# Kernel tuning notes

Measured on AMD Instinct MI355X. Metric: run time of the kernel, lower is better.

Reference implementation:

```python
import jax, jax.numpy as jnp
import numpy as np

N_ENTITIES = 100000
N_EDGES = 1250000
N_RELATIONS = 32
D = 64


def setup_inputs() -> dict:
    key = jax.random.key(0)
    k1, k2, k3, k4 = jax.random.split(key, 4)
    entity_emb = jax.random.normal(k1, (N_ENTITIES, D), dtype=jnp.float32)
    edge_index = jax.random.randint(k2, (2, N_EDGES), 0, N_ENTITIES, dtype=jnp.int64)
    edge_type = jax.random.randint(k3, (N_EDGES,), 0, N_RELATIONS, dtype=jnp.int64)
    weight = jax.random.normal(k4, (N_RELATIONS, D), dtype=jnp.float32)
    return {"entity_emb": entity_emb, "edge_index": edge_index,
            "edge_type": edge_type, "weight": weight}


def reference(entity_emb, edge_index, edge_type, weight):
    n_entities = entity_emb.shape[0]
    head, tail = edge_index[0], edge_index[1]
    # gather tail entity embeddings and relation embeddings, elementwise multiply
    neigh_relation_emb = entity_emb[tail] * weight[edge_type]  # [E, D]
    # scatter_mean by head index
    sums = jax.ops.segment_sum(neigh_relation_emb, head, num_segments=n_entities)
    counts = jax.ops.segment_sum(jnp.ones((head.shape[0],), dtype=entity_emb.dtype),
                                 head, num_segments=n_entities)
    entity_agg = sums / jnp.maximum(counts, 1.0)[:, None]  # empty segments -> 0
    return entity_agg
```

## Files before the change

### kernel.cpp

```cpp
#include <hip/hip_runtime.h>

#define D 64
#define BIN_SHIFT 7
#define BIN_SIZE 128
#define MAX_BINS 1024
#define BINCAP 2560
#define K1_THREADS 512
#define K1_EPT 10
#define K1_EPB (K1_THREADS * K1_EPT)
#define K2_THREADS 512
#define NREL 32


__device__ __forceinline__ float bf2f(unsigned short u) {
    union { unsigned i; float f; } x; x.i = ((unsigned)u) << 16; return x.f;
}

__global__ void cvt_kernel(const float* __restrict__ emb,
                           unsigned short* __restrict__ emb16,
                           int* __restrict__ binCount, int nbins, long n4) {
    long i = (long)blockIdx.x * blockDim.x + threadIdx.x;
    if (i < (long)nbins) binCount[i] = 0;
    if (i >= n4) return;
    float4 v = ((const float4*)emb)[i];
    ushort4 o;
    unsigned b;
    b = __float_as_uint(v.x); o.x = (unsigned short)((b + 0x7FFF + ((b >> 16) & 1)) >> 16);
    b = __float_as_uint(v.y); o.y = (unsigned short)((b + 0x7FFF + ((b >> 16) & 1)) >> 16);
    b = __float_as_uint(v.z); o.z = (unsigned short)((b + 0x7FFF + ((b >> 16) & 1)) >> 16);
    b = __float_as_uint(v.w); o.w = (unsigned short)((b + 0x7FFF + ((b >> 16) & 1)) >> 16);
    ((ushort4*)emb16)[i] = o;
}

__global__ void __launch_bounds__(K1_THREADS)
bin_sort_kernel(const int* __restrict__ head,
                const int* __restrict__ tail,
                const int* __restrict__ etype,
                int* __restrict__ binCount,
                unsigned* __restrict__ recs,
                int nbins, int n_edges) {
    __shared__ unsigned srec[K1_EPB];
    __shared__ int hist[MAX_BINS];
    __shared__ int base[MAX_BINS + 1];
    __shared__ int cur[MAX_BINS];
    __shared__ int gpos[MAX_BINS];
    __shared__ int tmp[K1_THREADS];
    __shared__ unsigned short binof[K1_EPB];

    int tid = threadIdx.x;
    for (int b = tid; b < MAX_BINS; b += K1_THREADS) hist[b] = 0;
    __syncthreads();

    long blockBase = (long)blockIdx.x * K1_EPB;
    int nvalid = (int)(((long)n_edges - blockBase < (long)K1_EPB)
                       ? ((long)n_edges - blockBase) : (long)K1_EPB);

    unsigned rv[K1_EPT]; int bv[K1_EPT];
#pragma unroll
    for (int k = 0; k < K1_EPT; k++) {
        long e = blockBase + (long)k * K1_THREADS + tid;
        if (e < n_edges) {
            int h = head[e];
            bv[k] = h >> BIN_SHIFT;
            rv[k] = (unsigned)tail[e] | ((unsigned)etype[e] << 17)
                  | ((unsigned)(h & (BIN_SIZE - 1)) << 22);
            atomicAdd(&hist[bv[k]], 1);
        } else bv[k] = -1;
    }
    __syncthreads();

    int s0 = hist[2 * tid], s1 = hist[2 * tid + 1];
    tmp[tid] = s0 + s1;
    __syncthreads();
    for (int s = 1; s < K1_THREADS; s <<= 1) {
        int x = (tid >= s) ? tmp[tid - s] : 0;
        __syncthreads();
        tmp[tid] += x;
        __syncthreads();
    }
    int pairExcl = tmp[tid] - (s0 + s1);
    base[2 * tid] = pairExcl;          cur[2 * tid] = pairExcl;
    base[2 * tid + 1] = pairExcl + s0; cur[2 * tid + 1] = pairExcl + s0;
    if (tid == K1_THREADS - 1) base[MAX_BINS] = tmp[tid];
    __syncthreads();

    for (int b = tid; b < nbins; b += K1_THREADS) {
        int c = hist[b];
        gpos[b] = (c > 0) ? atomicAdd(&binCount[b], c) : 0;
    }
    __syncthreads();

#pragma unroll
    for (int k = 0; k < K1_EPT; k++) {
        if (bv[k] >= 0) {
            int p = atomicAdd(&cur[bv[k]], 1);
            srec[p] = rv[k];
        }
    }
    __syncthreads();

    for (int b = tid; b < nbins; b += K1_THREADS) {
        int j0 = base[b], j1 = base[b + 1];
        for (int j = j0; j < j1; j++) binof[j] = (unsigned short)b;
    }
    __syncthreads();

    for (int i = tid; i < nvalid; i += K1_THREADS) {
        int b = binof[i];
        int off = gpos[b] + (i - base[b]);
        if (off < BINCAP)
            recs[(long)b * BINCAP + off] = srec[i];
    }
}

__global__ void __launch_bounds__(K2_THREADS)
aggregate_bin_kernel(const unsigned short* __restrict__ emb16,
                     const float* __restrict__ weight,
                     const unsigned* __restrict__ recs,
                     const int* __restrict__ binCount,
                     float* __restrict__ out, int n_ent) {
    __shared__ unsigned raw[BINCAP];
    __shared__ unsigned sorted[BINCAP + 16];
    __shared__ float wlds[NREL * D];
    __shared__ int hist[BIN_SIZE];
    __shared__ int off[BIN_SIZE];
    __shared__ int cur[BIN_SIZE];

    int tid = threadIdx.x;
    int b = blockIdx.x;
    int n = min(binCount[b], BINCAP);

    for (int i = tid; i < BINCAP + 16; i += K2_THREADS) sorted[i] = 0u;
    for (int i = tid; i < NREL * D; i += K2_THREADS) wlds[i] = weight[i];
    if (tid < BIN_SIZE) hist[tid] = 0;
    __syncthreads();

    const unsigned* gr = recs + (long)b * BINCAP;
    for (int i = tid; i < n; i += K2_THREADS) {
        unsigned q = gr[i];
        raw[i] = q;
        atomicAdd(&hist[(q >> 22) & 127], 1);
    }
    __syncthreads();

    int v = 0;
    if (tid < BIN_SIZE) { v = hist[tid]; off[tid] = v; }
    __syncthreads();
    for (int s = 1; s < BIN_SIZE; s <<= 1) {
        int x = 0;
        if (tid < BIN_SIZE && tid >= s) x = off[tid - s];
        __syncthreads();
        if (tid < BIN_SIZE) off[tid] += x;
        __syncthreads();
    }
    if (tid < BIN_SIZE) { off[tid] -= v; cur[tid] = off[tid]; }
    __syncthreads();

    for (int i = tid; i < n; i += K2_THREADS) {
        unsigned q = raw[i];
        int p = atomicAdd(&cur[(q >> 22) & 127], 1);
        sorted[p] = q;
    }
    __syncthreads();

    int lane = tid & 63;
    int wave = tid >> 6;
    int g = lane >> 4;
    int c = lane & 15;
    int hbase = b << BIN_SHIFT;

    for (int hl = wave; hl < BIN_SIZE; hl += 8) {
        if (hbase + hl >= n_ent) break;
        int o = off[hl];
        int deg = hist[hl];
        float4 acc = make_float4(0.f, 0.f, 0.f, 0.f);
        for (int i = 0; i < deg; i += 16) {
            int e0 = i + g, e1 = i + 4 + g, e2 = i + 8 + g, e3 = i + 12 + g;
            unsigned q0 = sorted[o + e0];
            unsigned q1 = sorted[o + e1];
            unsigned q2 = sorted[o + e2];
            unsigned q3 = sorted[o + e3];
            ushort4 u0 = *(const ushort4*)&emb16[(long)(q0 & 0x1FFFF) * D + c * 4];
            ushort4 u1 = *(const ushort4*)&emb16[(long)(q1 & 0x1FFFF) * D + c * 4];
            ushort4 u2 = *(const ushort4*)&emb16[(long)(q2 & 0x1FFFF) * D + c * 4];
            ushort4 u3 = *(const ushort4*)&emb16[(long)(q3 & 0x1FFFF) * D + c * 4];
            float4 w0 = *(const float4*)&wlds[(((q0 >> 17) & 31) << 6) + c * 4];
            float4 w1 = *(const float4*)&wlds[(((q1 >> 17) & 31) << 6) + c * 4];
            float4 w2 = *(const float4*)&wlds[(((q2 >> 17) & 31) << 6) + c * 4];
            float4 w3 = *(const float4*)&wlds[(((q3 >> 17) & 31) << 6) + c * 4];
            float m0 = (e0 < deg) ? 1.f : 0.f;
            float m1 = (e1 < deg) ? 1.f : 0.f;
            float m2 = (e2 < deg) ? 1.f : 0.f;
            float m3 = (e3 < deg) ? 1.f : 0.f;
            acc.x += m0 * bf2f(u0.x) * w0.x; acc.y += m0 * bf2f(u0.y) * w0.y;
            acc.z += m0 * bf2f(u0.z) * w0.z; acc.w += m0 * bf2f(u0.w) * w0.w;
            acc.x += m1 * bf2f(u1.x) * w1.x; acc.y += m1 * bf2f(u1.y) * w1.y;
            acc.z += m1 * bf2f(u1.z) * w1.z; acc.w += m1 * bf2f(u1.w) * w1.w;
            acc.x += m2 * bf2f(u2.x) * w2.x; acc.y += m2 * bf2f(u2.y) * w2.y;
            acc.z += m2 * bf2f(u2.z) * w2.z; acc.w += m2 * bf2f(u2.w) * w2.w;
            acc.x += m3 * bf2f(u3.x) * w3.x; acc.y += m3 * bf2f(u3.y) * w3.y;
            acc.z += m3 * bf2f(u3.z) * w3.z; acc.w += m3 * bf2f(u3.w) * w3.w;
        }
        acc.x += __shfl_xor(acc.x, 16); acc.y += __shfl_xor(acc.y, 16);
        acc.z += __shfl_xor(acc.z, 16); acc.w += __shfl_xor(acc.w, 16);
        acc.x += __shfl_xor(acc.x, 32); acc.y += __shfl_xor(acc.y, 32);
        acc.z += __shfl_xor(acc.z, 32); acc.w += __shfl_xor(acc.w, 32);
        if (g == 0) {
            float inv = 1.f / fmaxf((float)deg, 1.f);
            *(float4*)&out[(long)(hbase + hl) * D + c * 4] =
                make_float4(acc.x * inv, acc.y * inv, acc.z * inv, acc.w * inv);
        }
    }
}

__global__ void fb_scatter(const float* __restrict__ emb, const int* __restrict__ head,
                           const int* __restrict__ tail, const int* __restrict__ etype,
                           const float* __restrict__ weight, float* __restrict__ out,
                           float* __restrict__ cnt, int n_edges) {
    int gtid = blockIdx.x * blockDim.x + threadIdx.x;
    int e = gtid >> 6, lane = threadIdx.x & 63;
    if (e >= n_edges) return;
    int h = head[e], t = tail[e], r = etype[e];
    atomicAdd(&out[(long)h * D + lane], emb[(long)t * D + lane] * weight[r * D + lane]);
    if (lane == 0) atomicAdd(&cnt[h], 1.0f);
}
__global__ void fb_divide(float* __restrict__ out, const float* __restrict__ cnt, int n) {
    int i = blockIdx.x * blockDim.x + threadIdx.x;
    if (i < n) out[i] = out[i] / fmaxf(cnt[i >> 6], 1.0f);
}


extern "C" void kernel_launch(void* const* d_in, const int* in_sizes, int n_in,
                              void* d_out, int out_size, void* d_ws, size_t ws_size,
                              hipStream_t stream) {
    const float* emb    = (const float*)d_in[0];
    const int*   eidx   = (const int*)  d_in[1];
    const int*   etype  = (const int*)  d_in[2];
    const float* weight = (const float*)d_in[3];
    float* out = (float*)d_out;

    int n_edges = in_sizes[2];
    int n_ent   = out_size / D;
    const int* head = eidx;
    const int* tail = eidx + n_edges;

    int nbins = (n_ent + BIN_SIZE - 1) >> BIN_SHIFT;
    size_t recs_bytes = sizeof(int) * ((size_t)nbins * BINCAP);
    size_t cnt_bytes  = sizeof(int) * (size_t)nbins;
    size_t emb16_off  = (cnt_bytes + recs_bytes + 15) & ~((size_t)15);
    size_t need = emb16_off + (size_t)n_ent * D * sizeof(unsigned short);
    long mean_load = (n_ent > 0) ? ((long)n_edges * BIN_SIZE / n_ent) : 0;
    bool ok = (n_ent <= 131072) && (nbins <= MAX_BINS) && (ws_size >= need) &&
              (mean_load + 700 <= BINCAP);

    if (ok) {
        int* binCount  = (int*)d_ws;
        unsigned* recs = (unsigned*)(binCount + nbins);
        unsigned short* emb16 = (unsigned short*)((char*)d_ws + emb16_off);

        long n4 = (long)n_ent * D / 4;
        cvt_kernel<<<(int)((n4 + 255) / 256), 256, 0, stream>>>(
            emb, emb16, binCount, nbins, n4);

        int nblocks = (n_edges + K1_EPB - 1) / K1_EPB;
        bin_sort_kernel<<<nblocks, K1_THREADS, 0, stream>>>(
            head, tail, etype, binCount, recs, nbins, n_edges);

        aggregate_bin_kernel<<<nbins, K2_THREADS, 0, stream>>>(
            emb16, weight, recs, binCount, out, n_ent);
    } else {
        float* cnt = (float*)d_ws;
        hipMemsetAsync(out, 0, (size_t)out_size * sizeof(float), stream);
        hipMemsetAsync(cnt, 0, (size_t)n_ent * sizeof(float), stream);
        long tt = (long)n_edges * 64;
        fb_scatter<<<(int)((tt + 255) / 256), 256, 0, stream>>>(
            emb, head, tail, etype, weight, out, cnt, n_edges);
        fb_divide<<<(out_size + 255) / 256, 256, 0, stream>>>(out, cnt, out_size);
    }
}
```

Baseline: 152.5 us.

## Process two heads per wave, use wave-shuffle scan, trim LDS zeroing

The aggregation loop now has each wave handle two head nodes at once, issuing eight gathers per iteration instead of four, so more memory requests are in flight. The LDS prefix scan over the 128-entry histogram is replaced by a single-wave shuffle scan, removing the many block-wide barriers. Only the 16 padding slots after the valid records are zeroed instead of the whole sorted buffer, and launch bounds now request 4 blocks per CU. The costs are higher register pressure and wasted work when the two paired heads have unequal degrees.

```diff
diff --git a/kernel.cpp b/kernel.cpp
--- a/kernel.cpp
+++ b/kernel.cpp
@@ -113,7 +113,7 @@
     }
 }
 
-__global__ void __launch_bounds__(K2_THREADS)
+__global__ void __launch_bounds__(K2_THREADS, 4)
 aggregate_bin_kernel(const unsigned short* __restrict__ emb16,
                      const float* __restrict__ weight,
                      const unsigned* __restrict__ recs,
@@ -130,7 +130,7 @@
     int b = blockIdx.x;
     int n = min(binCount[b], BINCAP);
 
-    for (int i = tid; i < BINCAP + 16; i += K2_THREADS) sorted[i] = 0u;
+    if (tid < 16) sorted[n + tid] = 0u;
     for (int i = tid; i < NREL * D; i += K2_THREADS) wlds[i] = weight[i];
     if (tid < BIN_SIZE) hist[tid] = 0;
     __syncthreads();
@@ -143,17 +143,25 @@
     }
     __syncthreads();
 
-    int v = 0;
-    if (tid < BIN_SIZE) { v = hist[tid]; off[tid] = v; }
-    __syncthreads();
-    for (int s = 1; s < BIN_SIZE; s <<= 1) {
-        int x = 0;
-        if (tid < BIN_SIZE && tid >= s) x = off[tid - s];
-        __syncthreads();
-        if (tid < BIN_SIZE) off[tid] += x;
-        __syncthreads();
-    }
-    if (tid < BIN_SIZE) { off[tid] -= v; cur[tid] = off[tid]; }
+    int lane = tid & 63;
+    int wave = tid >> 6;
+
+    if (wave == 0) {
+        int h0 = hist[lane];
+        int h1 = hist[64 + lane];
+        int s0 = h0, s1 = h1;
+#pragma unroll
+        for (int s = 1; s < 64; s <<= 1) {
+            int t0 = __shfl_up(s0, s);
+            int t1 = __shfl_up(s1, s);
+            if (lane >= s) { s0 += t0; s1 += t1; }
+        }
+        int tot0 = __shfl(s0, 63);
+        int e0 = s0 - h0;
+        int e1 = tot0 + s1 - h1;
+        off[lane] = e0;      cur[lane] = e0;
+        off[64 + lane] = e1; cur[64 + lane] = e1;
+    }
     __syncthreads();
 
     for (int i = tid; i < n; i += K2_THREADS) {
@@ -163,52 +171,88 @@
     }
     __syncthreads();
 
-    int lane = tid & 63;
-    int wave = tid >> 6;
     int g = lane >> 4;
-    int c = lane & 15;
+    int c4 = (lane & 15) << 2;
     int hbase = b << BIN_SHIFT;
-
-    for (int hl = wave; hl < BIN_SIZE; hl += 8) {
-        if (hbase + hl >= n_ent) break;
-        int o = off[hl];
-        int deg = hist[hl];
-        float4 acc = make_float4(0.f, 0.f, 0.f, 0.f);
-        for (int i = 0; i < deg; i += 16) {
+    int nclamp = n + 15;
+
+#pragma unroll 1
+    for (int j = 0; j < 8; ++j) {
+        int hA = wave + (j << 4);
+        int hB = hA + 8;
+        int oA = off[hA], dA = hist[hA];
+        int oB = off[hB], dB = hist[hB];
+        int dmax = max(dA, dB);
+        float4 accA = make_float4(0.f, 0.f, 0.f, 0.f);
+        float4 accB = make_float4(0.f, 0.f, 0.f, 0.f);
+        for (int i = 0; i < dmax; i += 16) {
             int e0 = i + g, e1 = i + 4 + g, e2 = i + 8 + g, e3 = i + 12 + g;
-            unsigned q0 = sorted[o + e0];
-            unsigned q1 = sorted[o + e1];
-            unsigned q2 = sorted[o + e2];
-            unsigned q3 = sorted[o + e3];
-            ushort4 u0 = *(const ushort4*)&emb16[(long)(q0 & 0x1FFFF) * D + c * 4];
-            ushort4 u1 = *(const ushort4*)&emb16[(long)(q1 & 0x1FFFF) * D + c * 4];
-            ushort4 u2 = *(const ushort4*)&emb16[(long)(q2 & 0x1FFFF) * D + c * 4];
-            ushort4 u3 = *(const ushort4*)&emb16[(long)(q3 & 0x1FFFF) * D + c * 4];
-            float4 w0 = *(const float4*)&wlds[(((q0 >> 17) & 31) << 6) + c * 4];
-            float4 w1 = *(const float4*)&wlds[(((q1 >> 17) & 31) << 6) + c * 4];
-            float4 w2 = *(const float4*)&wlds[(((q2 >> 17) & 31) << 6) + c * 4];
-            float4 w3 = *(const float4*)&wlds[(((q3 >> 17) & 31) << 6) + c * 4];
-            float m0 = (e0 < deg) ? 1.f : 0.f;
-            float m1 = (e1 < deg) ? 1.f : 0.f;
-            float m2 = (e2 < deg) ? 1.f : 0.f;
-            float m3 = (e3 < deg) ? 1.f : 0.f;
-            acc.x += m0 * bf2f(u0.x) * w0.x; acc.y += m0 * bf2f(u0.y) * w0.y;
-            acc.z += m0 * bf2f(u0.z) * w0.z; acc.w += m0 * bf2f(u0.w) * w0.w;
-            acc.x += m1 * bf2f(u1.x) * w1.x; acc.y += m1 * bf2f(u1.y) * w1.y;
-            acc.z += m1 * bf2f(u1.z) * w1.z; acc.w += m1 * bf2f(u1.w) * w1.w;
-            acc.x += m2 * bf2f(u2.x) * w2.x; acc.y += m2 * bf2f(u2.y) * w2.y;
-            acc.z += m2 * bf2f(u2.z) * w2.z; acc.w += m2 * bf2f(u2.w) * w2.w;
-            acc.x += m3 * bf2f(u3.x) * w3.x; acc.y += m3 * bf2f(u3.y) * w3.y;
-            acc.z += m3 * bf2f(u3.z) * w3.z; acc.w += m3 * bf2f(u3.w) * w3.w;
-        }
-        acc.x += __shfl_xor(acc.x, 16); acc.y += __shfl_xor(acc.y, 16);
-        acc.z += __shfl_xor(acc.z, 16); acc.w += __shfl_xor(acc.w, 16);
-        acc.x += __shfl_xor(acc.x, 32); acc.y += __shfl_xor(acc.y, 32);
-        acc.z += __shfl_xor(acc.z, 32); acc.w += __shfl_xor(acc.w, 32);
-        if (g == 0) {
-            float inv = 1.f / fmaxf((float)deg, 1.f);
-            *(float4*)&out[(long)(hbase + hl) * D + c * 4] =
-                make_float4(acc.x * inv, acc.y * inv, acc.z * inv, acc.w * inv);
+            unsigned qa0 = sorted[min(oA + e0, nclamp)];
+            unsigned qa1 = sorted[min(oA + e1, nclamp)];
+            unsigned qa2 = sorted[min(oA + e2, nclamp)];
+            unsigned qa3 = sorted[min(oA + e3, nclamp)];
+            unsigned qb0 = sorted[min(oB + e0, nclamp)];
+            unsigned qb1 = sorted[min(oB + e1, nclamp)];
+            unsigned qb2 = sorted[min(oB + e2, nclamp)];
+            unsigned qb3 = sorted[min(oB + e3, nclamp)];
+            ushort4 ua0 = *(const ushort4*)&emb16[((long)(qa0 & 0x1FFFF) << 6) + c4];
+            ushort4 ua1 = *(const ushort4*)&emb16[((long)(qa1 & 0x1FFFF) << 6) + c4];
+            ushort4 ua2 = *(const ushort4*)&emb16[((long)(qa2 & 0x1FFFF) << 6) + c4];
+            ushort4 ua3 = *(const ushort4*)&emb16[((long)(qa3 & 0x1FFFF) << 6) + c4];
+            ushort4 ub0 = *(const ushort4*)&emb16[((long)(qb0 & 0x1FFFF) << 6) + c4];
+            ushort4 ub1 = *(const ushort4*)&emb16[((long)(qb1 & 0x1FFFF) << 6) + c4];
+            ushort4 ub2 = *(const ushort4*)&emb16[((long)(qb2 & 0x1FFFF) << 6) + c4];
+            ushort4 ub3 = *(const ushort4*)&emb16[((long)(qb3 & 0x1FFFF) << 6) + c4];
+            float4 wa0 = *(const float4*)&wlds[(((qa0 >> 17) & 31) << 6) + c4];
+            float4 wa1 = *(const float4*)&wlds[(((qa1 >> 17) & 31) << 6) + c4];
+            float4 wa2 = *(const float4*)&wlds[(((qa2 >> 17) & 31) << 6) + c4];
+            float4 wa3 = *(const float4*)&wlds[(((qa3 >> 17) & 31) << 6) + c4];
+            float4 wb0 = *(const float4*)&wlds[(((qb0 >> 17) & 31) << 6) + c4];
+            float4 wb1 = *(const float4*)&wlds[(((qb1 >> 17) & 31) << 6) + c4];
+            float4 wb2 = *(const float4*)&wlds[(((qb2 >> 17) & 31) << 6) + c4];
+            float4 wb3 = *(const float4*)&wlds[(((qb3 >> 17) & 31) << 6) + c4];
+            float ma0 = (e0 < dA) ? 1.f : 0.f;
+            float ma1 = (e1 < dA) ? 1.f : 0.f;
+            float ma2 = (e2 < dA) ? 1.f : 0.f;
+            float ma3 = (e3 < dA) ? 1.f : 0.f;
+            float mb0 = (e0 < dB) ? 1.f : 0.f;
+            float mb1 = (e1 < dB) ? 1.f : 0.f;
+            float mb2 = (e2 < dB) ? 1.f : 0.f;
+            float mb3 = (e3 < dB) ? 1.f : 0.f;
+            accA.x += ma0 * bf2f(ua0.x) * wa0.x; accA.y += ma0 * bf2f(ua0.y) * wa0.y;
+            accA.z += ma0 * bf2f(ua0.z) * wa0.z; accA.w += ma0 * bf2f(ua0.w) * wa0.w;
+            accA.x += ma1 * bf2f(ua1.x) * wa1.x; accA.y += ma1 * bf2f(ua1.y) * wa1.y;
+            accA.z += ma1 * bf2f(ua1.z) * wa1.z; accA.w += ma1 * bf2f(ua1.w) * wa1.w;
+            accA.x += ma2 * bf2f(ua2.x) * wa2.x; accA.y += ma2 * bf2f(ua2.y) * wa2.y;
+            accA.z += ma2 * bf2f(ua2.z) * wa2.z; accA.w += ma2 * bf2f(ua2.w) * wa2.w;
+            accA.x += ma3 * bf2f(ua3.x) * wa3.x; accA.y += ma3 * bf2f(ua3.y) * wa3.y;
+            accA.z += ma3 * bf2f(ua3.z) * wa3.z; accA.w += ma3 * bf2f(ua3.w) * wa3.w;
+            accB.x += mb0 * bf2f(ub0.x) * wb0.x; accB.y += mb0 * bf2f(ub0.y) * wb0.y;
+            accB.z += mb0 * bf2f(ub0.z) * wb0.z; accB.w += mb0 * bf2f(ub0.w) * wb0.w;
+            accB.x += mb1 * bf2f(ub1.x) * wb1.x; accB.y += mb1 * bf2f(ub1.y) * wb1.y;
+            accB.z += mb1 * bf2f(ub1.z) * wb1.z; accB.w += mb1 * bf2f(ub1.w) * wb1.w;
+            accB.x += mb2 * bf2f(ub2.x) * wb2.x; accB.y += mb2 * bf2f(ub2.y) * wb2.y;
+            accB.z += mb2 * bf2f(ub2.z) * wb2.z; accB.w += mb2 * bf2f(ub2.w) * wb2.w;
+            accB.x += mb3 * bf2f(ub3.x) * wb3.x; accB.y += mb3 * bf2f(ub3.y) * wb3.y;
+            accB.z += mb3 * bf2f(ub3.z) * wb3.z; accB.w += mb3 * bf2f(ub3.w) * wb3.w;
+        }
+        accA.x += __shfl_xor(accA.x, 16); accA.y += __shfl_xor(accA.y, 16);
+        accA.z += __shfl_xor(accA.z, 16); accA.w += __shfl_xor(accA.w, 16);
+        accA.x += __shfl_xor(accA.x, 32); accA.y += __shfl_xor(accA.y, 32);
+        accA.z += __shfl_xor(accA.z, 32); accA.w += __shfl_xor(accA.w, 32);
+        accB.x += __shfl_xor(accB.x, 16); accB.y += __shfl_xor(accB.y, 16);
+        accB.z += __shfl_xor(accB.z, 16); accB.w += __shfl_xor(accB.w, 16);
+        accB.x += __shfl_xor(accB.x, 32); accB.y += __shfl_xor(accB.y, 32);
+        accB.z += __shfl_xor(accB.z, 32); accB.w += __shfl_xor(accB.w, 32);
+        if (g == 0 && hbase + hA < n_ent) {
+            float inv = 1.f / fmaxf((float)dA, 1.f);
+            *(float4*)&out[((long)(hbase + hA) << 6) + c4] =
+                make_float4(accA.x * inv, accA.y * inv, accA.z * inv, accA.w * inv);
+        }
+        if (g == 0 && hbase + hB < n_ent) {
+            float inv = 1.f / fmaxf((float)dB, 1.f);
+            *(float4*)&out[((long)(hbase + hB) << 6) + c4] =
+                make_float4(accB.x * inv, accB.y * inv, accB.z * inv, accB.w * inv);
         }
     }
 }
```

Result: slower. 156.4 us (+2.6%).

## Software-pipeline head aggregation with double-buffered prefetch and wave-level scan

Applied to the files above, without the earlier changes.

The aggregation kernel now prefetches the first 16 edges' embedding and weight data for the next head while computing the current head, using two register sets A and B. This is meant to hide gather latency across heads. The 128-entry prefix scan now runs in a single wave with shuffles instead of a barrier-heavy LDS scan, and only the 16 tail slots of the sorted array are zeroed instead of the whole buffer. Launch bounds are set to request two blocks per CU. The extra live registers for the prefetch could raise register pressure or cause spills.

```diff
diff --git a/kernel.cpp b/kernel.cpp
--- a/kernel.cpp
+++ b/kernel.cpp
@@ -113,7 +113,7 @@
     }
 }
 
-__global__ void __launch_bounds__(K2_THREADS)
+__global__ void __launch_bounds__(K2_THREADS, 2)
 aggregate_bin_kernel(const unsigned short* __restrict__ emb16,
                      const float* __restrict__ weight,
                      const unsigned* __restrict__ recs,
@@ -130,7 +130,7 @@
     int b = blockIdx.x;
     int n = min(binCount[b], BINCAP);
 
-    for (int i = tid; i < BINCAP + 16; i += K2_THREADS) sorted[i] = 0u;
+    if (tid < 16) sorted[n + tid] = 0u;
     for (int i = tid; i < NREL * D; i += K2_THREADS) wlds[i] = weight[i];
     if (tid < BIN_SIZE) hist[tid] = 0;
     __syncthreads();
@@ -143,17 +143,25 @@
     }
     __syncthreads();
 
-    int v = 0;
-    if (tid < BIN_SIZE) { v = hist[tid]; off[tid] = v; }
-    __syncthreads();
-    for (int s = 1; s < BIN_SIZE; s <<= 1) {
-        int x = 0;
-        if (tid < BIN_SIZE && tid >= s) x = off[tid - s];
-        __syncthreads();
-        if (tid < BIN_SIZE) off[tid] += x;
-        __syncthreads();
-    }
-    if (tid < BIN_SIZE) { off[tid] -= v; cur[tid] = off[tid]; }
+    int lane = tid & 63;
+    int wave = tid >> 6;
+
+    if (wave == 0) {
+        int h0 = hist[lane];
+        int h1 = hist[64 + lane];
+        int s0 = h0, s1 = h1;
+#pragma unroll
+        for (int s = 1; s < 64; s <<= 1) {
+            int t0 = __shfl_up(s0, s);
+            int t1 = __shfl_up(s1, s);
+            if (lane >= s) { s0 += t0; s1 += t1; }
+        }
+        int tot0 = __shfl(s0, 63);
+        int e0 = s0 - h0;
+        int e1 = tot0 + s1 - h1;
+        off[lane] = e0;      cur[lane] = e0;
+        off[64 + lane] = e1; cur[64 + lane] = e1;
+    }
     __syncthreads();
 
     for (int i = tid; i < n; i += K2_THREADS) {
@@ -163,54 +171,105 @@
     }
     __syncthreads();
 
-    int lane = tid & 63;
-    int wave = tid >> 6;
     int g = lane >> 4;
-    int c = lane & 15;
+    int c4 = (lane & 15) << 2;
     int hbase = b << BIN_SHIFT;
 
-    for (int hl = wave; hl < BIN_SIZE; hl += 8) {
-        if (hbase + hl >= n_ent) break;
-        int o = off[hl];
-        int deg = hist[hl];
-        float4 acc = make_float4(0.f, 0.f, 0.f, 0.f);
-        for (int i = 0; i < deg; i += 16) {
-            int e0 = i + g, e1 = i + 4 + g, e2 = i + 8 + g, e3 = i + 12 + g;
-            unsigned q0 = sorted[o + e0];
-            unsigned q1 = sorted[o + e1];
-            unsigned q2 = sorted[o + e2];
-            unsigned q3 = sorted[o + e3];
-            ushort4 u0 = *(const ushort4*)&emb16[(long)(q0 & 0x1FFFF) * D + c * 4];
-            ushort4 u1 = *(const ushort4*)&emb16[(long)(q1 & 0x1FFFF) * D + c * 4];
-            ushort4 u2 = *(const ushort4*)&emb16[(long)(q2 & 0x1FFFF) * D + c * 4];
-            ushort4 u3 = *(const ushort4*)&emb16[(long)(q3 & 0x1FFFF) * D + c * 4];
-            float4 w0 = *(const float4*)&wlds[(((q0 >> 17) & 31) << 6) + c * 4];
-            float4 w1 = *(const float4*)&wlds[(((q1 >> 17) & 31) << 6) + c * 4];
-            float4 w2 = *(const float4*)&wlds[(((q2 >> 17) & 31) << 6) + c * 4];
-            float4 w3 = *(const float4*)&wlds[(((q3 >> 17) & 31) << 6) + c * 4];
-            float m0 = (e0 < deg) ? 1.f : 0.f;
-            float m1 = (e1 < deg) ? 1.f : 0.f;
-            float m2 = (e2 < deg) ? 1.f : 0.f;
-            float m3 = (e3 < deg) ? 1.f : 0.f;
-            acc.x += m0 * bf2f(u0.x) * w0.x; acc.y += m0 * bf2f(u0.y) * w0.y;
-            acc.z += m0 * bf2f(u0.z) * w0.z; acc.w += m0 * bf2f(u0.w) * w0.w;
-            acc.x += m1 * bf2f(u1.x) * w1.x; acc.y += m1 * bf2f(u1.y) * w1.y;
-            acc.z += m1 * bf2f(u1.z) * w1.z; acc.w += m1 * bf2f(u1.w) * w1.w;
-            acc.x += m2 * bf2f(u2.x) * w2.x; acc.y += m2 * bf2f(u2.y) * w2.y;
-            acc.z += m2 * bf2f(u2.z) * w2.z; acc.w += m2 * bf2f(u2.w) * w2.w;
-            acc.x += m3 * bf2f(u3.x) * w3.x; acc.y += m3 * bf2f(u3.y) * w3.y;
-            acc.z += m3 * bf2f(u3.z) * w3.z; acc.w += m3 * bf2f(u3.w) * w3.w;
-        }
-        acc.x += __shfl_xor(acc.x, 16); acc.y += __shfl_xor(acc.y, 16);
-        acc.z += __shfl_xor(acc.z, 16); acc.w += __shfl_xor(acc.w, 16);
-        acc.x += __shfl_xor(acc.x, 32); acc.y += __shfl_xor(acc.y, 32);
-        acc.z += __shfl_xor(acc.z, 32); acc.w += __shfl_xor(acc.w, 32);
-        if (g == 0) {
-            float inv = 1.f / fmaxf((float)deg, 1.f);
-            *(float4*)&out[(long)(hbase + hl) * D + c * 4] =
-                make_float4(acc.x * inv, acc.y * inv, acc.z * inv, acc.w * inv);
-        }
-    }
+    int oA, dA, oB, dB;
+    unsigned qa0, qa1, qa2, qa3, qb0, qb1, qb2, qb3;
+    ushort4 ua0, ua1, ua2, ua3, ub0, ub1, ub2, ub3;
+    float4 wa0, wa1, wa2, wa3, wb0, wb1, wb2, wb3;
+
+#define K2_PREF(J, o_, d_, q0, q1, q2, q3, u0, u1, u2, u3, w0, w1, w2, w3)    \
+    do {                                                                       \
+        int hh_ = wave + ((J) << 3);                                           \
+        o_ = off[hh_]; d_ = hist[hh_];                                         \
+        q0 = sorted[o_ + g];      q1 = sorted[o_ + 4 + g];                     \
+        q2 = sorted[o_ + 8 + g];  q3 = sorted[o_ + 12 + g];                    \
+        q0 = (g < d_)      ? q0 : 0u;                                          \
+        q1 = (4 + g < d_)  ? q1 : 0u;                                          \
+        q2 = (8 + g < d_)  ? q2 : 0u;                                          \
+        q3 = (12 + g < d_) ? q3 : 0u;                                          \
+        u0 = *(const ushort4*)&emb16[((long)(q0 & 0x1FFFF) << 6) + c4];        \
+        u1 = *(const ushort4*)&emb16[((long)(q1 & 0x1FFFF) << 6) + c4];        \
+        u2 = *(const ushort4*)&emb16[((long)(q2 & 0x1FFFF) << 6) + c4];        \
+        u3 = *(const ushort4*)&emb16[((long)(q3 & 0x1FFFF) << 6) + c4];        \
+        w0 = *(const float4*)&wlds[(((q0 >> 17) & 31) << 6) + c4];             \
+        w1 = *(const float4*)&wlds[(((q1 >> 17) & 31) << 6) + c4];             \
+        w2 = *(const float4*)&wlds[(((q2 >> 17) & 31) << 6) + c4];             \
+        w3 = *(const float4*)&wlds[(((q3 >> 17) & 31) << 6) + c4];             \
+    } while (0)
+
+#define K2_COMP(J, o_, d_, q0, q1, q2, q3, u0, u1, u2, u3, w0, w1, w2, w3)    \
+    do {                                                                       \
+        int hh_ = wave + ((J) << 3);                                           \
+        float4 acc = make_float4(0.f, 0.f, 0.f, 0.f);                          \
+        float m0 = (g < d_)      ? 1.f : 0.f;                                  \
+        float m1 = (4 + g < d_)  ? 1.f : 0.f;                                  \
+        float m2 = (8 + g < d_)  ? 1.f : 0.f;                                  \
+        float m3 = (12 + g < d_) ? 1.f : 0.f;                                  \
+        acc.x += m0 * bf2f(u0.x) * w0.x; acc.y += m0 * bf2f(u0.y) * w0.y;      \
+        acc.z += m0 * bf2f(u0.z) * w0.z; acc.w += m0 * bf2f(u0.w) * w0.w;      \
+        acc.x += m1 * bf2f(u1.x) * w1.x; acc.y += m1 * bf2f(u1.y) * w1.y;      \
+        acc.z += m1 * bf2f(u1.z) * w1.z; acc.w += m1 * bf2f(u1.w) * w1.w;      \
+        acc.x += m2 * bf2f(u2.x) * w2.x; acc.y += m2 * bf2f(u2.y) * w2.y;      \
+        acc.z += m2 * bf2f(u2.z) * w2.z; acc.w += m2 * bf2f(u2.w) * w2.w;      \
+        acc.x += m3 * bf2f(u3.x) * w3.x; acc.y += m3 * bf2f(u3.y) * w3.y;      \
+        acc.z += m3 * bf2f(u3.z) * w3.z; acc.w += m3 * bf2f(u3.w) * w3.w;      \
+        for (int i_ = 16; i_ < d_; i_ += 16) {          \
+            int e0_ = i_ + g, e1_ = i_ + 4 + g, e2_ = i_ + 8 + g,              \
+                e3_ = i_ + 12 + g;                                             \
+            unsigned t0 = sorted[o_ + e0_]; unsigned t1 = sorted[o_ + e1_];    \
+            unsigned t2 = sorted[o_ + e2_]; unsigned t3 = sorted[o_ + e3_];    \
+            t0 = (e0_ < d_) ? t0 : 0u;  t1 = (e1_ < d_) ? t1 : 0u;             \
+            t2 = (e2_ < d_) ? t2 : 0u;  t3 = (e3_ < d_) ? t3 : 0u;             \
+            ushort4 v0 = *(const ushort4*)&emb16[((long)(t0 & 0x1FFFF) << 6) + c4]; \
+            ushort4 v1 = *(const ushort4*)&emb16[((long)(t1 & 0x1FFFF) << 6) + c4]; \
+            ushort4 v2 = *(const ushort4*)&emb16[((long)(t2 & 0x1FFFF) << 6) + c4]; \
+            ushort4 v3 = *(const ushort4*)&emb16[((long)(t3 & 0x1FFFF) << 6) + c4]; \
+            float4 x0 = *(const float4*)&wlds[(((t0 >> 17) & 31) << 6) + c4];  \
+            float4 x1 = *(const float4*)&wlds[(((t1 >> 17) & 31) << 6) + c4];  \
+            float4 x2 = *(const float4*)&wlds[(((t2 >> 17) & 31) << 6) + c4];  \
+            float4 x3 = *(const float4*)&wlds[(((t3 >> 17) & 31) << 6) + c4];  \
+            float n0 = (e0_ < d_) ? 1.f : 0.f;                                 \
+            float n1 = (e1_ < d_) ? 1.f : 0.f;                                 \
+            float n2 = (e2_ < d_) ? 1.f : 0.f;                                 \
+            float n3 = (e3_ < d_) ? 1.f : 0.f;                                 \
+            acc.x += n0 * bf2f(v0.x) * x0.x; acc.y += n0 * bf2f(v0.y) * x0.y;  \
+            acc.z += n0 * bf2f(v0.z) * x0.z; acc.w += n0 * bf2f(v0.w) * x0.w;  \
+            acc.x += n1 * bf2f(v1.x) * x1.x; acc.y += n1 * bf2f(v1.y) * x1.y;  \
+            acc.z += n1 * bf2f(v1.z) * x1.z; acc.w += n1 * bf2f(v1.w) * x1.w;  \
+            acc.x += n2 * bf2f(v2.x) * x2.x; acc.y += n2 * bf2f(v2.y) * x2.y;  \
+            acc.z += n2 * bf2f(v2.z) * x2.z; acc.w += n2 * bf2f(v2.w) * x2.w;  \
+            acc.x += n3 * bf2f(v3.x) * x3.x; acc.y += n3 * bf2f(v3.y) * x3.y;  \
+            acc.z += n3 * bf2f(v3.z) * x3.z; acc.w += n3 * bf2f(v3.w) * x3.w;  \
+        }                                                                      \
+        acc.x += __shfl_xor(acc.x, 16); acc.y += __shfl_xor(acc.y, 16);        \
+        acc.z += __shfl_xor(acc.z, 16); acc.w += __shfl_xor(acc.w, 16);        \
+        acc.x += __shfl_xor(acc.x, 32); acc.y += __shfl_xor(acc.y, 32);        \
+        acc.z += __shfl_xor(acc.z, 32); acc.w += __shfl_xor(acc.w, 32);        \
+        if (g == 0 && hbase + hh_ < n_ent) {                                   \
+            float inv = 1.f / fmaxf((float)d_, 1.f);                           \
+            *(float4*)&out[((long)(hbase + hh_) << 6) + c4] =                  \
+                make_float4(acc.x * inv, acc.y * inv, acc.z * inv, acc.w * inv);\
+        }                                                                      \
+    } while (0)
+
+    K2_PREF(0, oA, dA, qa0, qa1, qa2, qa3, ua0, ua1, ua2, ua3, wa0, wa1, wa2, wa3);
+#pragma unroll 1
+    for (int j = 0; j < 16; j += 2) {
+        K2_PREF(j + 1, oB, dB, qb0, qb1, qb2, qb3, ub0, ub1, ub2, ub3,
+                wb0, wb1, wb2, wb3);
+        K2_COMP(j, oA, dA, qa0, qa1, qa2, qa3, ua0, ua1, ua2, ua3,
+                wa0, wa1, wa2, wa3);
+        int jn = (j + 2 < 16) ? (j + 2) : 15;
+        K2_PREF(jn, oA, dA, qa0, qa1, qa2, qa3, ua0, ua1, ua2, ua3,
+                wa0, wa1, wa2, wa3);
+        K2_COMP(j + 1, oB, dB, qb0, qb1, qb2, qb3, ub0, ub1, ub2, ub3,
+                wb0, wb1, wb2, wb3);
+    }
+#undef K2_PREF
+#undef K2_COMP
 }
 
 __global__ void fb_scatter(const float* __restrict__ emb, const int* __restrict__ head,
```

Measured after the change: 146.7 us. 1.04x faster.
